# Performance work log

Measured on AMD Instinct MI355X. Metric: run time of the kernel, lower is better.

## Reference

```python
import jax, jax.numpy as jnp
import numpy as np
import math

B, S, H, D = 2, 2048, 16, 64

def setup_inputs() -> dict:
    key = jax.random.key(0)
    ks = jax.random.split(key, 9)
    s = 1.0 / math.sqrt(D)
    return {
        "query": jax.random.normal(ks[0], (B, S, H, D), jnp.float32),
        "key": jax.random.normal(ks[1], (B, S, H, D), jnp.float32),
        "value": jax.random.normal(ks[2], (B, S, H, D), jnp.float32),
        "Wq": jax.random.normal(ks[3], (D, D), jnp.float32) * s,
        "bq": jax.random.normal(ks[4], (D,), jnp.float32) * 0.01,
        "Wk": jax.random.normal(ks[5], (D, D), jnp.float32) * s,
        "bk": jax.random.normal(ks[6], (D,), jnp.float32) * 0.01,
        "Wv": jax.random.normal(ks[7], (D, D), jnp.float32) * s,
        "bv": jax.random.normal(ks[8], (D,), jnp.float32) * 0.01,
    }

def reference(query, key, value, Wq, bq, Wk, bk, Wv, bv):
    # Linear projections on last dim (torch Linear: x @ W.T + b)
    q = query @ Wq.T + bq          # [B, S, H, D]
    k = key @ Wk.T + bk
    v = value @ Wv.T + bv
    # permute(0,2,1,3) -> [B, H, S, D]
    q = jnp.transpose(q, (0, 2, 1, 3))
    k = jnp.transpose(k, (0, 2, 1, 3))
    v = jnp.transpose(v, (0, 2, 1, 3))
    q = q / math.sqrt(q.shape[-1])
    # scaled QK^T, cast to fp32 (as in source), softmax, cast to fp16
    scores = jnp.einsum('bhqd,bhkd->bhqk', q, k).astype(jnp.float32)
    attn = jax.nn.softmax(scores, axis=-1).astype(jnp.float16)
    # fp16 attn @ fp32 v (jax promotes to fp32)
    out = jnp.einsum('bhqk,bhkd->bhqd', attn, v)
    return out
```

## Files before the change

### kernel.cpp

```cpp
#include <hip/hip_runtime.h>

#define B_ 2
#define S_ 2048
#define H_ 16
#define D_ 64
#define QBLK 64
#define KBLK 64

typedef _Float16 f16x8 __attribute__((ext_vector_type(8)));
typedef float f32x4 __attribute__((ext_vector_type(4)));

__device__ inline f16x8 cvt8(const float* p) {
    float4 u = *(const float4*)p, v = *(const float4*)(p + 4);
    f16x8 r;
    r[0] = (_Float16)u.x; r[1] = (_Float16)u.y; r[2] = (_Float16)u.z; r[3] = (_Float16)u.w;
    r[4] = (_Float16)v.x; r[5] = (_Float16)v.y; r[6] = (_Float16)v.z; r[7] = (_Float16)v.w;
    return r;
}

__global__ __launch_bounds__(256) void proj_kernel(
    const float* __restrict__ query, const float* __restrict__ key,
    const float* __restrict__ value,
    const float* __restrict__ Wq, const float* __restrict__ bq,
    const float* __restrict__ Wk, const float* __restrict__ bk,
    const float* __restrict__ Wv, const float* __restrict__ bv,
    _Float16* __restrict__ qo, _Float16* __restrict__ ko, _Float16* __restrict__ vo)
{
    const int which = blockIdx.z;
    const float* x    = which == 0 ? query : (which == 1 ? key : value);
    const float* W    = which == 0 ? Wq    : (which == 1 ? Wk  : Wv);
    const float* bias = which == 0 ? bq    : (which == 1 ? bk  : bv);
    _Float16*    out  = which == 0 ? qo    : (which == 1 ? ko  : vo);
    const float scale = which == 0 ? 0.125f : 1.0f;

    const int bh = blockIdx.y;
    const int b  = bh >> 4, h = bh & 15;
    const int s0 = blockIdx.x * 64;

    const int t = threadIdx.x;
    const int wave = t >> 6, lane = t & 63;
    const int lg = lane >> 4, lr = lane & 15;

    const float* xrow = x + ((long)((b * S_ + s0 + wave * 16 + lr)) * H_ + h) * 64;
    f16x8 a[2];
    a[0] = cvt8(xrow + 0 * 32 + lg * 8);
    a[1] = cvt8(xrow + 1 * 32 + lg * 8);

    f32x4 acc[4] = {};
    #pragma unroll
    for (int jb = 0; jb < 4; ++jb) {
        #pragma unroll
        for (int kc = 0; kc < 2; ++kc) {
            f16x8 bf = cvt8(W + (jb * 16 + lr) * 64 + kc * 32 + lg * 8);
            acc[jb] = __builtin_amdgcn_mfma_f32_16x16x32_f16(a[kc], bf, acc[jb], 0, 0, 0);
        }
    }

    const long orow = (long)bh * S_ + s0 + wave * 16;
    #pragma unroll
    for (int jb = 0; jb < 4; ++jb) {
        float bj = bias[jb * 16 + lr];
        #pragma unroll
        for (int r = 0; r < 4; ++r) {
            out[(orow + lg * 4 + r) * 64 + jb * 16 + lr] =
                (_Float16)((acc[jb][r] + bj) * scale);
        }
    }
}

__global__ __launch_bounds__(256) void transpose_v(
    const _Float16* __restrict__ in, _Float16* __restrict__ out)
{
    __shared__ _Float16 tile[64 * 64];
    const int bh = blockIdx.y;
    const int st = blockIdx.x * 64;
    const _Float16* src = in + ((long)bh * S_ + st) * 64;
    const int t = threadIdx.x;

    #pragma unroll
    for (int idx = t; idx < 512; idx += 256) {
        int s = idx >> 3, c = idx & 7;
        uint4 v = *(const uint4*)(src + s * 64 + c * 8);
        int byte = (s * 128 + c * 16) ^ ((s & 7) << 4);
        *(uint4*)((char*)tile + byte) = v;
    }
    __syncthreads();

    const int d = t >> 2, seg = t & 3;
    _Float16 pack[16];
    #pragma unroll
    for (int i = 0; i < 16; ++i) {
        int ii = (i + seg * 4) & 15;
        int s = seg * 16 + ii;
        int byte = (s * 128 + d * 2) ^ ((s & 7) << 4);
        pack[ii] = *(const _Float16*)((const char*)tile + byte);
    }
    _Float16* dst = out + ((long)bh * 64 + d) * S_ + st + seg * 16;
    *(uint4*)(dst)     = *(uint4*)(pack);
    *(uint4*)(dst + 8) = *(uint4*)(pack + 8);
}

__global__ __launch_bounds__(256) void attn_kernel(
    const _Float16* __restrict__ Qg, const _Float16* __restrict__ Kg,
    const _Float16* __restrict__ Vtg, float* __restrict__ Og)
{
    __shared__ _Float16 Kt[64 * 64];
    __shared__ _Float16 Vt[64 * 64];
    __shared__ _Float16 Pl[4][16 * 64];

    const int bh = blockIdx.x;
    const int qt = blockIdx.y;
    const _Float16* Qb = Qg  + (long)bh * S_ * 64;
    const _Float16* Kb = Kg  + (long)bh * S_ * 64;
    const _Float16* Vb = Vtg + (long)bh * 64 * S_;

    const int t = threadIdx.x;
    const int wave = t >> 6, lane = t & 63;
    const int lg = lane >> 4, lr = lane & 15;

    f16x8 qf[2];
    {
        const _Float16* qrow = Qb + ((long)(qt * QBLK + wave * 16 + lr)) * 64;
        qf[0] = *(const f16x8*)(qrow + 0 * 32 + lg * 8);
        qf[1] = *(const f16x8*)(qrow + 1 * 32 + lg * 8);
    }

    f32x4 o[4] = {};
    float m[4], l_[4];
    #pragma unroll
    for (int r = 0; r < 4; ++r) { m[r] = -1e30f; l_[r] = 0.f; }

    for (int kt = 0; kt < S_ / KBLK; ++kt) {
        __syncthreads();
        {
            const _Float16* src = Kb + (long)kt * KBLK * 64;
            #pragma unroll
            for (int idx = t; idx < 512; idx += 256) {
                int row = idx >> 3, c = idx & 7;
                uint4 v = *(const uint4*)(src + row * 64 + c * 8);
                int byte = (row * 128 + c * 16) ^ ((row & 7) << 4);
                *(uint4*)((char*)Kt + byte) = v;
            }
            #pragma unroll
            for (int idx = t; idx < 512; idx += 256) {
                int row = idx >> 3, c = idx & 7;
                uint4 v = *(const uint4*)(Vb + (long)row * S_ + kt * KBLK + c * 8);
                int byte = (row * 128 + c * 16) ^ ((row & 7) << 4);
                *(uint4*)((char*)Vt + byte) = v;
            }
        }
        __syncthreads();

        f32x4 sc[4];
        #pragma unroll
        for (int f = 0; f < 4; ++f) {
            f32x4 acc = {};
            #pragma unroll
            for (int kc = 0; kc < 2; ++kc) {
                int row = f * 16 + lr;
                int byte = (row * 128 + (kc * 32 + lg * 8) * 2) ^ ((row & 7) << 4);
                f16x8 bfr = *(const f16x8*)((const char*)Kt + byte);
                acc = __builtin_amdgcn_mfma_f32_16x16x32_f16(qf[kc], bfr, acc, 0, 0, 0);
            }
            sc[f] = acc;
        }

        float pm[4];
        #pragma unroll
        for (int r = 0; r < 4; ++r)
            pm[r] = fmaxf(fmaxf(sc[0][r], sc[1][r]), fmaxf(sc[2][r], sc[3][r]));
        #pragma unroll
        for (int off = 1; off < 16; off <<= 1) {
            #pragma unroll
            for (int r = 0; r < 4; ++r) pm[r] = fmaxf(pm[r], __shfl_xor(pm[r], off));
        }
        float mn[4], rs[4];
        #pragma unroll
        for (int r = 0; r < 4; ++r) {
            mn[r] = fmaxf(m[r], pm[r]);
            rs[r] = __expf(m[r] - mn[r]);
            m[r]  = mn[r];
            l_[r] *= rs[r];
        }
        #pragma unroll
        for (int db = 0; db < 4; ++db)
            #pragma unroll
            for (int r = 0; r < 4; ++r) o[db][r] *= rs[r];

        char* pbase = (char*)&Pl[wave][0];
        #pragma unroll
        for (int f = 0; f < 4; ++f) {
            #pragma unroll
            for (int r = 0; r < 4; ++r) {
                float p = __expf(sc[f][r] - mn[r]);
                l_[r] += p;
                int R = lg * 4 + r;
                int byte = (R * 128 + (f * 16 + lr) * 2) ^ ((R & 7) << 4);
                *(_Float16*)(pbase + byte) = (_Float16)p;
            }
        }

        f16x8 pa[2];
        #pragma unroll
        for (int kc = 0; kc < 2; ++kc) {
            int pbyte = (lr * 128 + (kc * 32 + lg * 8) * 2) ^ ((lr & 7) << 4);
            pa[kc] = *(const f16x8*)(pbase + pbyte);
        }
        #pragma unroll
        for (int db = 0; db < 4; ++db) {
            #pragma unroll
            for (int kc = 0; kc < 2; ++kc) {
                int vrow = db * 16 + lr;
                int vbyte = (vrow * 128 + (kc * 32 + lg * 8) * 2) ^ ((vrow & 7) << 4);
                f16x8 vb = *(const f16x8*)((const char*)Vt + vbyte);
                o[db] = __builtin_amdgcn_mfma_f32_16x16x32_f16(pa[kc], vb, o[db], 0, 0, 0);
            }
        }
    }

    #pragma unroll
    for (int off = 1; off < 16; off <<= 1) {
        #pragma unroll
        for (int r = 0; r < 4; ++r) l_[r] += __shfl_xor(l_[r], off);
    }
    float inv[4];
    #pragma unroll
    for (int r = 0; r < 4; ++r) inv[r] = 1.0f / l_[r];

    const long obase = ((long)bh * S_ + qt * QBLK + wave * 16) * 64;
    #pragma unroll
    for (int db = 0; db < 4; ++db) {
        #pragma unroll
        for (int r = 0; r < 4; ++r) {
            int R = lg * 4 + r;
            int d = db * 16 + lr;
            Og[obase + (long)R * 64 + d] = o[db][r] * inv[r];
        }
    }
}

extern "C" void kernel_launch(void* const* d_in, const int* in_sizes, int n_in,
                              void* d_out, int out_size, void* d_ws, size_t ws_size,
                              hipStream_t stream) {
    const float* query = (const float*)d_in[0];
    const float* key   = (const float*)d_in[1];
    const float* value = (const float*)d_in[2];
    const float* Wq    = (const float*)d_in[3];
    const float* bq    = (const float*)d_in[4];
    const float* Wk    = (const float*)d_in[5];
    const float* bk    = (const float*)d_in[6];
    const float* Wv    = (const float*)d_in[7];
    const float* bv    = (const float*)d_in[8];

    const size_t elems = (size_t)B_ * H_ * S_ * D_;
    _Float16* qws  = (_Float16*)d_ws;
    _Float16* kws  = qws + elems;
    _Float16* vws  = kws + elems;
    _Float16* vtws = vws + elems;

    proj_kernel<<<dim3(S_ / 64, B_ * H_, 3), 256, 0, stream>>>(
        query, key, value, Wq, bq, Wk, bk, Wv, bv, qws, kws, vws);

    transpose_v<<<dim3(S_ / 64, B_ * H_), 256, 0, stream>>>(vws, vtws);

    attn_kernel<<<dim3(B_ * H_, S_ / QBLK), 256, 0, stream>>>(
        qws, kws, vtws, (float*)d_out);
}
```

Measured before the change: 233.9 us.

## Rewrite attention with 32x32 MFMA, register softmax, and fused V transpose

Folds the V transpose into the projection kernel, which now writes V directly in transposed layout, removing one launch. The attention kernel drops LDS staging and reads K and V straight from global memory into registers. It computes S^T with 32x32x16 MFMAs at 128 queries per block and passes P through lane shuffles instead of shared memory. It also uses exp2 with log2e folded into the Q scale, skips rescaling when the running max grows by at most 10, and raises wave priority around the MFMAs. The tradeoffs are no cross-wave reuse of K and V through LDS, strided stores into the transposed V, and an approximate lazy rescale threshold.

```diff
diff --git a/kernel.cpp b/kernel.cpp
--- a/kernel.cpp
+++ b/kernel.cpp
@@ -4,17 +4,23 @@
 #define S_ 2048
 #define H_ 16
 #define D_ 64
-#define QBLK 64
-#define KBLK 64
-
+
+typedef _Float16 f16;
 typedef _Float16 f16x8 __attribute__((ext_vector_type(8)));
 typedef float f32x4 __attribute__((ext_vector_type(4)));
+typedef float f32x16 __attribute__((ext_vector_type(16)));
+
+#define LOG2E 1.44269504088896f
+
+__device__ inline unsigned int pk16(float a, float b) {
+    return __builtin_bit_cast(unsigned int, __builtin_amdgcn_cvt_pkrtz(a, b));
+}
 
 __device__ inline f16x8 cvt8(const float* p) {
     float4 u = *(const float4*)p, v = *(const float4*)(p + 4);
     f16x8 r;
-    r[0] = (_Float16)u.x; r[1] = (_Float16)u.y; r[2] = (_Float16)u.z; r[3] = (_Float16)u.w;
-    r[4] = (_Float16)v.x; r[5] = (_Float16)v.y; r[6] = (_Float16)v.z; r[7] = (_Float16)v.w;
+    r[0] = (f16)u.x; r[1] = (f16)u.y; r[2] = (f16)u.z; r[3] = (f16)u.w;
+    r[4] = (f16)v.x; r[5] = (f16)v.y; r[6] = (f16)v.z; r[7] = (f16)v.w;
     return r;
 }
 
@@ -24,14 +30,13 @@
     const float* __restrict__ Wq, const float* __restrict__ bq,
     const float* __restrict__ Wk, const float* __restrict__ bk,
     const float* __restrict__ Wv, const float* __restrict__ bv,
-    _Float16* __restrict__ qo, _Float16* __restrict__ ko, _Float16* __restrict__ vo)
+    f16* __restrict__ qo, f16* __restrict__ ko, f16* __restrict__ vto)
 {
     const int which = blockIdx.z;
     const float* x    = which == 0 ? query : (which == 1 ? key : value);
     const float* W    = which == 0 ? Wq    : (which == 1 ? Wk  : Wv);
     const float* bias = which == 0 ? bq    : (which == 1 ? bk  : bv);
-    _Float16*    out  = which == 0 ? qo    : (which == 1 ? ko  : vo);
-    const float scale = which == 0 ? 0.125f : 1.0f;
+    const float scale = which == 0 ? 0.125f * LOG2E : 1.0f;
 
     const int bh = blockIdx.y;
     const int b  = bh >> 4, h = bh & 15;
@@ -56,186 +61,139 @@
         }
     }
 
-    const long orow = (long)bh * S_ + s0 + wave * 16;
+    if (which == 2) {
+        #pragma unroll
+        for (int jb = 0; jb < 4; ++jb) {
+            float bj = bias[jb * 16 + lr];
+            int d = jb * 16 + lr;
+            #pragma unroll
+            for (int r = 0; r < 4; ++r) {
+                int s = s0 + wave * 16 + lg * 4 + r;
+                vto[((long)bh * 64 + d) * S_ + s] = (f16)(acc[jb][r] + bj);
+            }
+        }
+    } else {
+        f16* out = which == 0 ? qo : ko;
+        const long orow = (long)bh * S_ + s0 + wave * 16;
+        #pragma unroll
+        for (int jb = 0; jb < 4; ++jb) {
+            float bj = bias[jb * 16 + lr];
+            #pragma unroll
+            for (int r = 0; r < 4; ++r) {
+                out[(orow + lg * 4 + r) * 64 + jb * 16 + lr] =
+                    (f16)((acc[jb][r] + bj) * scale);
+            }
+        }
+    }
+}
+
+__global__ __launch_bounds__(256) void attn_kernel(
+    const f16* __restrict__ Qg, const f16* __restrict__ Kg,
+    const f16* __restrict__ Vtg, float* __restrict__ Og)
+{
+    const int bid = blockIdx.x;
+    const int bh = bid & 31;
+    const int qt = bid >> 5;
+    const int warp = threadIdx.x >> 6;
+    const int lane = threadIdx.x & 63;
+    const int hi = lane >> 5;
+    const int lq = lane & 31;
+    const int q0 = qt * 128 + warp * 32;
+
+    const f16* Qb = Qg  + ((long)bh * S_ + q0) * 64;
+    const f16* Kb = Kg  + (long)bh * S_ * 64;
+    const f16* Vt = Vtg + (long)bh * 64 * S_;
+
+    f16x8 qf[4];
     #pragma unroll
-    for (int jb = 0; jb < 4; ++jb) {
-        float bj = bias[jb * 16 + lr];
-        #pragma unroll
-        for (int r = 0; r < 4; ++r) {
-            out[(orow + lg * 4 + r) * 64 + jb * 16 + lr] =
-                (_Float16)((acc[jb][r] + bj) * scale);
-        }
-    }
-}
-
-__global__ __launch_bounds__(256) void transpose_v(
-    const _Float16* __restrict__ in, _Float16* __restrict__ out)
-{
-    __shared__ _Float16 tile[64 * 64];
-    const int bh = blockIdx.y;
-    const int st = blockIdx.x * 64;
-    const _Float16* src = in + ((long)bh * S_ + st) * 64;
-    const int t = threadIdx.x;
-
+    for (int ks = 0; ks < 4; ++ks)
+        qf[ks] = *(const f16x8*)(Qb + (long)lq * 64 + ks * 16 + hi * 8);
+
+    f32x16 o0 = {}, o1 = {};
+    float m = -1e30f, l = 0.f;
+
+    for (int kt = 0; kt < S_ / 64; ++kt) {
+        const f16* Kt = Kb + kt * 64 * 64;
+        const f16* Vk = Vt + kt * 64;
+
+        f32x16 s0 = {}, s1 = {};
+        #pragma unroll
+        for (int ks = 0; ks < 4; ++ks) {
+            f16x8 k0 = *(const f16x8*)(Kt + (lq)      * 64 + ks * 16 + hi * 8);
+            f16x8 k1 = *(const f16x8*)(Kt + (32 + lq) * 64 + ks * 16 + hi * 8);
+            __builtin_amdgcn_s_setprio(1);
+            s0 = __builtin_amdgcn_mfma_f32_32x32x16_f16(k0, qf[ks], s0, 0, 0, 0);
+            s1 = __builtin_amdgcn_mfma_f32_32x32x16_f16(k1, qf[ks], s1, 0, 0, 0);
+            __builtin_amdgcn_s_setprio(0);
+        }
+
+        f16x8 vf[8];
+        #pragma unroll
+        for (int db = 0; db < 2; ++db)
+            #pragma unroll
+            for (int ks = 0; ks < 4; ++ks)
+                vf[db * 4 + ks] = *(const f16x8*)(Vk + (long)(db * 32 + lq) * S_ + ks * 16 + hi * 8);
+
+        float pm = s0[0];
+        #pragma unroll
+        for (int r = 1; r < 16; ++r) pm = fmaxf(pm, s0[r]);
+        #pragma unroll
+        for (int r = 0; r < 16; ++r) pm = fmaxf(pm, s1[r]);
+        pm = fmaxf(pm, __shfl_xor(pm, 32));
+
+        if (!__all(pm <= m + 10.0f)) {
+            float mn = fmaxf(m, pm);
+            float rs = exp2f(m - mn);
+            #pragma unroll
+            for (int r = 0; r < 16; ++r) { o0[r] *= rs; o1[r] *= rs; }
+            l *= rs;
+            m = mn;
+        }
+
+        float sum = 0.f;
+        #pragma unroll
+        for (int r = 0; r < 16; ++r) { s0[r] = exp2f(s0[r] - m); sum += s0[r]; }
+        #pragma unroll
+        for (int r = 0; r < 16; ++r) { s1[r] = exp2f(s1[r] - m); sum += s1[r]; }
+        l += sum;
+
+        unsigned int w[16], xw[16];
+        #pragma unroll
+        for (int i = 0; i < 8; ++i) {
+            w[i]     = pk16(s0[2 * i], s0[2 * i + 1]);
+            w[8 + i] = pk16(s1[2 * i], s1[2 * i + 1]);
+        }
+        #pragma unroll
+        for (int i = 0; i < 16; ++i) xw[i] = __shfl_xor(w[i], 32);
+
+        union PA { unsigned int u[4]; f16x8 v; };
+        PA pa[4];
+        #pragma unroll
+        for (int ks = 0; ks < 4; ++ks) {
+            int bse = (ks >> 1) * 8 + (ks & 1) * 4;
+            pa[ks].u[0] = hi ? xw[bse + 2] : w[bse + 0];
+            pa[ks].u[1] = hi ? xw[bse + 3] : w[bse + 1];
+            pa[ks].u[2] = hi ? w[bse + 2]  : xw[bse + 0];
+            pa[ks].u[3] = hi ? w[bse + 3]  : xw[bse + 1];
+        }
+
+        __builtin_amdgcn_s_setprio(1);
+        #pragma unroll
+        for (int ks = 0; ks < 4; ++ks) {
+            o0 = __builtin_amdgcn_mfma_f32_32x32x16_f16(vf[ks],     pa[ks].v, o0, 0, 0, 0);
+            o1 = __builtin_amdgcn_mfma_f32_32x32x16_f16(vf[4 + ks], pa[ks].v, o1, 0, 0, 0);
+        }
+        __builtin_amdgcn_s_setprio(0);
+    }
+
+    float lt = l + __shfl_xor(l, 32);
+    float inv = 1.0f / lt;
+    float* orow = Og + ((long)bh * S_ + q0 + lq) * 64;
     #pragma unroll
-    for (int idx = t; idx < 512; idx += 256) {
-        int s = idx >> 3, c = idx & 7;
-        uint4 v = *(const uint4*)(src + s * 64 + c * 8);
-        int byte = (s * 128 + c * 16) ^ ((s & 7) << 4);
-        *(uint4*)((char*)tile + byte) = v;
-    }
-    __syncthreads();
-
-    const int d = t >> 2, seg = t & 3;
-    _Float16 pack[16];
-    #pragma unroll
-    for (int i = 0; i < 16; ++i) {
-        int ii = (i + seg * 4) & 15;
-        int s = seg * 16 + ii;
-        int byte = (s * 128 + d * 2) ^ ((s & 7) << 4);
-        pack[ii] = *(const _Float16*)((const char*)tile + byte);
-    }
-    _Float16* dst = out + ((long)bh * 64 + d) * S_ + st + seg * 16;
-    *(uint4*)(dst)     = *(uint4*)(pack);
-    *(uint4*)(dst + 8) = *(uint4*)(pack + 8);
-}
-
-__global__ __launch_bounds__(256) void attn_kernel(
-    const _Float16* __restrict__ Qg, const _Float16* __restrict__ Kg,
-    const _Float16* __restrict__ Vtg, float* __restrict__ Og)
-{
-    __shared__ _Float16 Kt[64 * 64];
-    __shared__ _Float16 Vt[64 * 64];
-    __shared__ _Float16 Pl[4][16 * 64];
-
-    const int bh = blockIdx.x;
-    const int qt = blockIdx.y;
-    const _Float16* Qb = Qg  + (long)bh * S_ * 64;
-    const _Float16* Kb = Kg  + (long)bh * S_ * 64;
-    const _Float16* Vb = Vtg + (long)bh * 64 * S_;
-
-    const int t = threadIdx.x;
-    const int wave = t >> 6, lane = t & 63;
-    const int lg = lane >> 4, lr = lane & 15;
-
-    f16x8 qf[2];
-    {
-        const _Float16* qrow = Qb + ((long)(qt * QBLK + wave * 16 + lr)) * 64;
-        qf[0] = *(const f16x8*)(qrow + 0 * 32 + lg * 8);
-        qf[1] = *(const f16x8*)(qrow + 1 * 32 + lg * 8);
-    }
-
-    f32x4 o[4] = {};
-    float m[4], l_[4];
-    #pragma unroll
-    for (int r = 0; r < 4; ++r) { m[r] = -1e30f; l_[r] = 0.f; }
-
-    for (int kt = 0; kt < S_ / KBLK; ++kt) {
-        __syncthreads();
-        {
-            const _Float16* src = Kb + (long)kt * KBLK * 64;
-            #pragma unroll
-            for (int idx = t; idx < 512; idx += 256) {
-                int row = idx >> 3, c = idx & 7;
-                uint4 v = *(const uint4*)(src + row * 64 + c * 8);
-                int byte = (row * 128 + c * 16) ^ ((row & 7) << 4);
-                *(uint4*)((char*)Kt + byte) = v;
-            }
-            #pragma unroll
-            for (int idx = t; idx < 512; idx += 256) {
-                int row = idx >> 3, c = idx & 7;
-                uint4 v = *(const uint4*)(Vb + (long)row * S_ + kt * KBLK + c * 8);
-                int byte = (row * 128 + c * 16) ^ ((row & 7) << 4);
-                *(uint4*)((char*)Vt + byte) = v;
-            }
-        }
-        __syncthreads();
-
-        f32x4 sc[4];
-        #pragma unroll
-        for (int f = 0; f < 4; ++f) {
-            f32x4 acc = {};
-            #pragma unroll
-            for (int kc = 0; kc < 2; ++kc) {
-                int row = f * 16 + lr;
-                int byte = (row * 128 + (kc * 32 + lg * 8) * 2) ^ ((row & 7) << 4);
-                f16x8 bfr = *(const f16x8*)((const char*)Kt + byte);
-                acc = __builtin_amdgcn_mfma_f32_16x16x32_f16(qf[kc], bfr, acc, 0, 0, 0);
-            }
-            sc[f] = acc;
-        }
-
-        float pm[4];
-        #pragma unroll
-        for (int r = 0; r < 4; ++r)
-            pm[r] = fmaxf(fmaxf(sc[0][r], sc[1][r]), fmaxf(sc[2][r], sc[3][r]));
-        #pragma unroll
-        for (int off = 1; off < 16; off <<= 1) {
-            #pragma unroll
-            for (int r = 0; r < 4; ++r) pm[r] = fmaxf(pm[r], __shfl_xor(pm[r], off));
-        }
-        float mn[4], rs[4];
-        #pragma unroll
-        for (int r = 0; r < 4; ++r) {
-            mn[r] = fmaxf(m[r], pm[r]);
-            rs[r] = __expf(m[r] - mn[r]);
-            m[r]  = mn[r];
-            l_[r] *= rs[r];
-        }
-        #pragma unroll
-        for (int db = 0; db < 4; ++db)
-            #pragma unroll
-            for (int r = 0; r < 4; ++r) o[db][r] *= rs[r];
-
-        char* pbase = (char*)&Pl[wave][0];
-        #pragma unroll
-        for (int f = 0; f < 4; ++f) {
-            #pragma unroll
-            for (int r = 0; r < 4; ++r) {
-                float p = __expf(sc[f][r] - mn[r]);
-                l_[r] += p;
-                int R = lg * 4 + r;
-                int byte = (R * 128 + (f * 16 + lr) * 2) ^ ((R & 7) << 4);
-                *(_Float16*)(pbase + byte) = (_Float16)p;
-            }
-        }
-
-        f16x8 pa[2];
-        #pragma unroll
-        for (int kc = 0; kc < 2; ++kc) {
-            int pbyte = (lr * 128 + (kc * 32 + lg * 8) * 2) ^ ((lr & 7) << 4);
-            pa[kc] = *(const f16x8*)(pbase + pbyte);
-        }
-        #pragma unroll
-        for (int db = 0; db < 4; ++db) {
-            #pragma unroll
-            for (int kc = 0; kc < 2; ++kc) {
-                int vrow = db * 16 + lr;
-                int vbyte = (vrow * 128 + (kc * 32 + lg * 8) * 2) ^ ((vrow & 7) << 4);
-                f16x8 vb = *(const f16x8*)((const char*)Vt + vbyte);
-                o[db] = __builtin_amdgcn_mfma_f32_16x16x32_f16(pa[kc], vb, o[db], 0, 0, 0);
-            }
-        }
-    }
-
-    #pragma unroll
-    for (int off = 1; off < 16; off <<= 1) {
-        #pragma unroll
-        for (int r = 0; r < 4; ++r) l_[r] += __shfl_xor(l_[r], off);
-    }
-    float inv[4];
-    #pragma unroll
-    for (int r = 0; r < 4; ++r) inv[r] = 1.0f / l_[r];
-
-    const long obase = ((long)bh * S_ + qt * QBLK + wave * 16) * 64;
-    #pragma unroll
-    for (int db = 0; db < 4; ++db) {
-        #pragma unroll
-        for (int r = 0; r < 4; ++r) {
-            int R = lg * 4 + r;
-            int d = db * 16 + lr;
-            Og[obase + (long)R * 64 + d] = o[db][r] * inv[r];
-        }
+    for (int r = 0; r < 16; ++r) {
+        int d0 = (r & 3) + 8 * (r >> 2) + 4 * hi;
+        orow[d0]      = o0[r] * inv;
+        orow[d0 + 32] = o1[r] * inv;
     }
 }
 
@@ -253,16 +211,12 @@
     const float* bv    = (const float*)d_in[8];
 
     const size_t elems = (size_t)B_ * H_ * S_ * D_;
-    _Float16* qws  = (_Float16*)d_ws;
-    _Float16* kws  = qws + elems;
-    _Float16* vws  = kws + elems;
-    _Float16* vtws = vws + elems;
+    f16* qws  = (f16*)d_ws;
+    f16* kws  = qws + elems;
+    f16* vtws = kws + elems;
 
     proj_kernel<<<dim3(S_ / 64, B_ * H_, 3), 256, 0, stream>>>(
-        query, key, value, Wq, bq, Wk, bk, Wv, bv, qws, kws, vws);
-
-    transpose_v<<<dim3(S_ / 64, B_ * H_), 256, 0, stream>>>(vws, vtws);
-
-    attn_kernel<<<dim3(B_ * H_, S_ / QBLK), 256, 0, stream>>>(
-        qws, kws, vtws, (float*)d_out);
-}
+        query, key, value, Wq, bq, Wk, bk, Wv, bv, qws, kws, vtws);
+
+    attn_kernel<<<512, 256, 0, stream>>>(qws, kws, vtws, (float*)d_out);
+}
```

Result: slower. 246.1 us (+5.2%).
